# Kernel tuning notes

Hardware: AMD Instinct MI355X
Metric: run time of the kernel (lower is better)

Reference implementation:

```python
import jax, jax.numpy as jnp
import numpy as np

B, H, S = 64, 1024, 512
MIN_VAL, MAX_VAL = -1.0, 1.0
EPS = 1e-8  # torch F.cosine_similarity default eps


def setup_inputs() -> dict:
    key = jax.random.key(0)
    k1, k2, k3 = jax.random.split(key, 3)
    tree_state = jax.random.normal(k1, (B, H), dtype=jnp.float32)
    seq_states = jax.random.normal(k2, (B, H, S), dtype=jnp.float32)
    # binary validity mask (float, as it is multiplied in)
    seq_mask = (jax.random.uniform(k3, (B, S)) < 0.9).astype(jnp.float32)
    return {"tree_state": tree_state, "seq_states": seq_states, "seq_mask": seq_mask}


def reference(tree_state, seq_states, seq_mask):
    # scan over the seq axis; carry h: (B, H)
    xs = (jnp.transpose(seq_states, (2, 0, 1)), seq_mask.T)  # (S,B,H), (S,B)

    def step(h, x):
        s, m = x  # s: (B,H), m: (B,)
        dot = jnp.sum(h * s, axis=-1)  # (B,)
        denom = jnp.maximum(
            jnp.linalg.norm(h, axis=-1) * jnp.linalg.norm(s, axis=-1), EPS
        )
        cos = (dot / denom)[:, None]  # (B,1)
        h_new = jnp.clip(h + (s - h * cos) * m[:, None], MIN_VAL, MAX_VAL)
        return h_new, None

    h, _ = jax.lax.scan(step, tree_state, xs)
    return h
```

## Files before the change

### kernel.cpp

```cpp
#include <hip/hip_runtime.h>


#define NB 64
#define NH 1024
#define NS 512
#define EL 16

template <int CTRL>
__device__ __forceinline__ float dpp_add(float x) {
  int s = __builtin_amdgcn_update_dpp(0, __builtin_bit_cast(int, x), CTRL, 0xf,
                                      0xf, true);
  return x + __builtin_bit_cast(float, s);
}

__device__ __forceinline__ float readlane_f(float v, int lane) {
  return __builtin_bit_cast(
      float, __builtin_amdgcn_readlane(__builtin_bit_cast(int, v), lane));
}

__device__ __forceinline__ void wave_sum3(float& a, float& b, float& c) {
  a = dpp_add<0x111>(a); b = dpp_add<0x111>(b); c = dpp_add<0x111>(c);
  a = dpp_add<0x112>(a); b = dpp_add<0x112>(b); c = dpp_add<0x112>(c);
  a = dpp_add<0x114>(a); b = dpp_add<0x114>(b); c = dpp_add<0x114>(c);
  a = dpp_add<0x118>(a); b = dpp_add<0x118>(b); c = dpp_add<0x118>(c);
  a = dpp_add<0x142>(a); b = dpp_add<0x142>(b); c = dpp_add<0x142>(c);
  a = dpp_add<0x143>(a); b = dpp_add<0x143>(b); c = dpp_add<0x143>(c);
  a = readlane_f(a, 63);
  b = readlane_f(b, 63);
  c = readlane_f(c, 63);
}

__global__ __launch_bounds__(64, 1) void otsu_scan_kernel(
    const float* __restrict__ tree,
    const float* __restrict__ seq,
    const float* __restrict__ mask,
    float* __restrict__ out) {
  const int b = blockIdx.x;
  const int lane = threadIdx.x;

  const float* hrow = tree + b * NH + lane * EL;
  float h[EL];
#pragma unroll
  for (int i = 0; i < EL / 4; ++i) {
    float4 v = *(const float4*)(hrow + 4 * i);
    h[4 * i + 0] = v.x;
    h[4 * i + 1] = v.y;
    h[4 * i + 2] = v.z;
    h[4 * i + 3] = v.w;
  }

  float m8[8];
#pragma unroll
  for (int k = 0; k < 8; ++k) m8[k] = mask[b * NS + k * 64 + lane];

  const float* srow = seq + (size_t)b * NH * NS + (size_t)(lane * EL) * NS;

  float bufA[4 * EL], bufB[4 * EL];

  auto prefetch = [&](float* buf, int g) {
    const float* p = srow + 4 * g;
#pragma unroll
    for (int i = 0; i < EL; ++i) {
      float4 v = *(const float4*)(p + i * NS);
      buf[4 * i + 0] = v.x;
      buf[4 * i + 1] = v.y;
      buf[4 * i + 2] = v.z;
      buf[4 * i + 3] = v.w;
    }
    __builtin_amdgcn_sched_barrier(0);
  };

  auto full_step = [&](const float* buf, int j) {
    float d0 = 0.f, d1 = 0.f, d2 = 0.f, d3 = 0.f;
    float e0 = 0.f, e1 = 0.f, e2 = 0.f, e3 = 0.f;
    float f0 = 0.f, f1 = 0.f, f2 = 0.f, f3 = 0.f;
#pragma unroll
    for (int i = 0; i < EL; i += 4) {
      const float s0 = buf[4 * (i + 0) + j];
      const float s1 = buf[4 * (i + 1) + j];
      const float s2v = buf[4 * (i + 2) + j];
      const float s3 = buf[4 * (i + 3) + j];
      d0 = fmaf(h[i + 0], s0, d0);
      d1 = fmaf(h[i + 1], s1, d1);
      d2 = fmaf(h[i + 2], s2v, d2);
      d3 = fmaf(h[i + 3], s3, d3);
      e0 = fmaf(h[i + 0], h[i + 0], e0);
      e1 = fmaf(h[i + 1], h[i + 1], e1);
      e2 = fmaf(h[i + 2], h[i + 2], e2);
      e3 = fmaf(h[i + 3], h[i + 3], e3);
      f0 = fmaf(s0, s0, f0);
      f1 = fmaf(s1, s1, f1);
      f2 = fmaf(s2v, s2v, f2);
      f3 = fmaf(s3, s3, f3);
    }
    float dot = (d0 + d1) + (d2 + d3);
    float h2 = (e0 + e1) + (e2 + e3);
    float s2 = (f0 + f1) + (f2 + f3);
    wave_sum3(dot, h2, s2);
    const float denom = fmaxf(__builtin_amdgcn_sqrtf(h2 * s2), 1e-8f);
    const float c = dot * __builtin_amdgcn_rcpf(denom);
    const float a = 1.0f - c;
#pragma unroll
    for (int i = 0; i < EL; ++i) {
      h[i] = __builtin_amdgcn_fmed3f(fmaf(h[i], a, buf[4 * i + j]), -1.0f,
                                     1.0f);
    }
  };

  auto process = [&](const float* buf, float mvec, int lbase, bool has_t0) {
#pragma unroll
    for (int j = 0; j < 4; ++j) {
      const float m = readlane_f(mvec, lbase + j);
      if (m != 0.0f) {
        full_step(buf, j);
      } else if (has_t0 && j == 0) {
#pragma unroll
        for (int i = 0; i < EL; ++i)
          h[i] = __builtin_amdgcn_fmed3f(h[i], -1.0f, 1.0f);
      }
    }
  };

  prefetch(bufA, 0);

#pragma unroll
  for (int sg = 0; sg < 8; ++sg) {
    const float mvec = m8[sg];
    for (int gg = 0; gg < 16; gg += 2) {
      const int g = sg * 16 + gg;
      prefetch(bufB, g + 1);
      process(bufA, mvec, 4 * gg, sg == 0 && gg == 0);
      if (g + 2 < NS / 4) prefetch(bufA, g + 2);
      process(bufB, mvec, 4 * gg + 4, false);
    }
  }

  float* orow = out + b * NH + lane * EL;
#pragma unroll
  for (int i = 0; i < EL / 4; ++i) {
    float4 v;
    v.x = h[4 * i + 0];
    v.y = h[4 * i + 1];
    v.z = h[4 * i + 2];
    v.w = h[4 * i + 3];
    *(float4*)(orow + 4 * i) = v;
  }
}

extern "C" void kernel_launch(void* const* d_in, const int* in_sizes, int n_in,
                              void* d_out, int out_size, void* d_ws,
                              size_t ws_size, hipStream_t stream) {
  const float* tree = (const float*)d_in[0];
  const float* seq = (const float*)d_in[1];
  const float* mask = (const float*)d_in[2];
  float* out = (float*)d_out;
  otsu_scan_kernel<<<dim3(NB), dim3(64), 0, stream>>>(tree, seq, mask, out);
}
```

Before: 321.2 us.

## Hand-schedule global loads with inline asm and batch seq-norm reductions per group

Replaces compiler-generated prefetch with inline-asm dwordx4 loads carrying immediate offsets and explicit vmcnt waits, so one buffer's loads stay in flight while the other is processed. The squared norms of the four seq columns in a group are computed together and reduced in one four-way DPP reduction, taking that reduction off the per-step serial chain; each step now reduces only dot and |h|^2. The sqrt-plus-reciprocal becomes a single rsq with the eps clamp squared. The risks are fragile manual waitcnt accounting and a slightly different eps and rounding behaviour.

```diff
diff --git a/kernel.cpp b/kernel.cpp
--- a/kernel.cpp
+++ b/kernel.cpp
@@ -5,6 +5,8 @@
 #define NH 1024
 #define NS 512
 #define EL 16
+
+typedef float v4f __attribute__((ext_vector_type(4)));
 
 template <int CTRL>
 __device__ __forceinline__ float dpp_add(float x) {
@@ -18,17 +20,70 @@
       float, __builtin_amdgcn_readlane(__builtin_bit_cast(int, v), lane));
 }
 
-__device__ __forceinline__ void wave_sum3(float& a, float& b, float& c) {
-  a = dpp_add<0x111>(a); b = dpp_add<0x111>(b); c = dpp_add<0x111>(c);
-  a = dpp_add<0x112>(a); b = dpp_add<0x112>(b); c = dpp_add<0x112>(c);
-  a = dpp_add<0x114>(a); b = dpp_add<0x114>(b); c = dpp_add<0x114>(c);
-  a = dpp_add<0x118>(a); b = dpp_add<0x118>(b); c = dpp_add<0x118>(c);
-  a = dpp_add<0x142>(a); b = dpp_add<0x142>(b); c = dpp_add<0x142>(c);
-  a = dpp_add<0x143>(a); b = dpp_add<0x143>(b); c = dpp_add<0x143>(c);
+__device__ __forceinline__ void wave_sum2(float& a, float& b) {
+  a = dpp_add<0x111>(a); b = dpp_add<0x111>(b);
+  a = dpp_add<0x112>(a); b = dpp_add<0x112>(b);
+  a = dpp_add<0x114>(a); b = dpp_add<0x114>(b);
+  a = dpp_add<0x118>(a); b = dpp_add<0x118>(b);
+  a = dpp_add<0x142>(a); b = dpp_add<0x142>(b);
+  a = dpp_add<0x143>(a); b = dpp_add<0x143>(b);
+  a = readlane_f(a, 63);
+  b = readlane_f(b, 63);
+}
+
+__device__ __forceinline__ void wave_sum4(float& a, float& b, float& c,
+                                          float& d) {
+  a = dpp_add<0x111>(a); b = dpp_add<0x111>(b); c = dpp_add<0x111>(c); d = dpp_add<0x111>(d);
+  a = dpp_add<0x112>(a); b = dpp_add<0x112>(b); c = dpp_add<0x112>(c); d = dpp_add<0x112>(d);
+  a = dpp_add<0x114>(a); b = dpp_add<0x114>(b); c = dpp_add<0x114>(c); d = dpp_add<0x114>(d);
+  a = dpp_add<0x118>(a); b = dpp_add<0x118>(b); c = dpp_add<0x118>(c); d = dpp_add<0x118>(d);
+  a = dpp_add<0x142>(a); b = dpp_add<0x142>(b); c = dpp_add<0x142>(c); d = dpp_add<0x142>(d);
+  a = dpp_add<0x143>(a); b = dpp_add<0x143>(b); c = dpp_add<0x143>(c); d = dpp_add<0x143>(d);
   a = readlane_f(a, 63);
   b = readlane_f(b, 63);
   c = readlane_f(c, 63);
-}
+  d = readlane_f(d, 63);
+}
+
+#define GLD4(dst, p, OFFSTR)                                   \
+  asm volatile("global_load_dwordx4 %0, %1, off" OFFSTR        \
+               : "=v"(dst)                                     \
+               : "v"(p))
+#define GLD1(dst, p)                                           \
+  asm volatile("global_load_dword %0, %1, off" : "=v"(dst) : "v"(p))
+
+#define ISSUE16(buf)                       \
+  do {                                     \
+    GLD4(buf[0], p0, " offset:-4096");     \
+    GLD4(buf[1], p0, " offset:-2048");     \
+    GLD4(buf[2], p0, "");                  \
+    GLD4(buf[3], p0, " offset:2048");      \
+    GLD4(buf[4], p1, " offset:-4096");     \
+    GLD4(buf[5], p1, " offset:-2048");     \
+    GLD4(buf[6], p1, "");                  \
+    GLD4(buf[7], p1, " offset:2048");      \
+    GLD4(buf[8], p2, " offset:-4096");     \
+    GLD4(buf[9], p2, " offset:-2048");     \
+    GLD4(buf[10], p2, "");                 \
+    GLD4(buf[11], p2, " offset:2048");     \
+    GLD4(buf[12], p3, " offset:-4096");    \
+    GLD4(buf[13], p3, " offset:-2048");    \
+    GLD4(buf[14], p3, "");                 \
+    GLD4(buf[15], p3, " offset:2048");     \
+    p0 += 4; p1 += 4; p2 += 4; p3 += 4;    \
+  } while (0)
+
+#define WAITPIN(buf, N)                                             \
+  do {                                                              \
+    asm volatile("s_waitcnt vmcnt(" N ")"                           \
+                 : "+v"(buf[0]), "+v"(buf[1]), "+v"(buf[2]),        \
+                   "+v"(buf[3]), "+v"(buf[4]), "+v"(buf[5]),        \
+                   "+v"(buf[6]), "+v"(buf[7]));                     \
+    asm volatile("s_waitcnt vmcnt(" N ")"                           \
+                 : "+v"(buf[8]), "+v"(buf[9]), "+v"(buf[10]),       \
+                   "+v"(buf[11]), "+v"(buf[12]), "+v"(buf[13]),     \
+                   "+v"(buf[14]), "+v"(buf[15]));                   \
+  } while (0)
 
 __global__ __launch_bounds__(64, 1) void otsu_scan_kernel(
     const float* __restrict__ tree,
@@ -39,80 +94,97 @@
   const int lane = threadIdx.x;
 
   const float* hrow = tree + b * NH + lane * EL;
+  v4f hv[4];
+  GLD4(hv[0], hrow, "");
+  GLD4(hv[1], hrow, " offset:16");
+  GLD4(hv[2], hrow, " offset:32");
+  GLD4(hv[3], hrow, " offset:48");
+  float m8[8];
+  {
+    const float* mp = mask + b * NS + lane;
+    GLD1(m8[0], mp);
+    GLD1(m8[1], mp + 64);
+    GLD1(m8[2], mp + 128);
+    GLD1(m8[3], mp + 192);
+    GLD1(m8[4], mp + 256);
+    GLD1(m8[5], mp + 320);
+    GLD1(m8[6], mp + 384);
+    GLD1(m8[7], mp + 448);
+  }
+  asm volatile("s_waitcnt vmcnt(0)"
+               : "+v"(hv[0]), "+v"(hv[1]), "+v"(hv[2]), "+v"(hv[3]),
+                 "+v"(m8[0]), "+v"(m8[1]), "+v"(m8[2]), "+v"(m8[3]),
+                 "+v"(m8[4]), "+v"(m8[5]), "+v"(m8[6]), "+v"(m8[7]));
+
   float h[EL];
 #pragma unroll
-  for (int i = 0; i < EL / 4; ++i) {
-    float4 v = *(const float4*)(hrow + 4 * i);
-    h[4 * i + 0] = v.x;
-    h[4 * i + 1] = v.y;
-    h[4 * i + 2] = v.z;
-    h[4 * i + 3] = v.w;
-  }
-
-  float m8[8];
-#pragma unroll
-  for (int k = 0; k < 8; ++k) m8[k] = mask[b * NS + k * 64 + lane];
+  for (int k = 0; k < 4; ++k) {
+    h[4 * k + 0] = hv[k].x;
+    h[4 * k + 1] = hv[k].y;
+    h[4 * k + 2] = hv[k].z;
+    h[4 * k + 3] = hv[k].w;
+  }
 
   const float* srow = seq + (size_t)b * NH * NS + (size_t)(lane * EL) * NS;
-
-  float bufA[4 * EL], bufB[4 * EL];
-
-  auto prefetch = [&](float* buf, int g) {
-    const float* p = srow + 4 * g;
-#pragma unroll
-    for (int i = 0; i < EL; ++i) {
-      float4 v = *(const float4*)(p + i * NS);
-      buf[4 * i + 0] = v.x;
-      buf[4 * i + 1] = v.y;
-      buf[4 * i + 2] = v.z;
-      buf[4 * i + 3] = v.w;
+  const float* p0 = srow + 2 * NS;
+  const float* p1 = srow + 6 * NS;
+  const float* p2 = srow + 10 * NS;
+  const float* p3 = srow + 14 * NS;
+
+  v4f bufA[16], bufB[16];
+
+  auto process4 = [&](const v4f* buf, float mv, int lbase, bool has_t0) {
+    float fA0 = 0.f, fA1 = 0.f, fA2 = 0.f, fA3 = 0.f;
+    float fB0 = 0.f, fB1 = 0.f, fB2 = 0.f, fB3 = 0.f;
+#pragma unroll
+    for (int i = 0; i < EL; i += 2) {
+      fA0 = fmaf(buf[i][0], buf[i][0], fA0);
+      fA1 = fmaf(buf[i][1], buf[i][1], fA1);
+      fA2 = fmaf(buf[i][2], buf[i][2], fA2);
+      fA3 = fmaf(buf[i][3], buf[i][3], fA3);
+      fB0 = fmaf(buf[i + 1][0], buf[i + 1][0], fB0);
+      fB1 = fmaf(buf[i + 1][1], buf[i + 1][1], fB1);
+      fB2 = fmaf(buf[i + 1][2], buf[i + 1][2], fB2);
+      fB3 = fmaf(buf[i + 1][3], buf[i + 1][3], fB3);
     }
-    __builtin_amdgcn_sched_barrier(0);
-  };
-
-  auto full_step = [&](const float* buf, int j) {
-    float d0 = 0.f, d1 = 0.f, d2 = 0.f, d3 = 0.f;
-    float e0 = 0.f, e1 = 0.f, e2 = 0.f, e3 = 0.f;
-    float f0 = 0.f, f1 = 0.f, f2 = 0.f, f3 = 0.f;
-#pragma unroll
-    for (int i = 0; i < EL; i += 4) {
-      const float s0 = buf[4 * (i + 0) + j];
-      const float s1 = buf[4 * (i + 1) + j];
-      const float s2v = buf[4 * (i + 2) + j];
-      const float s3 = buf[4 * (i + 3) + j];
-      d0 = fmaf(h[i + 0], s0, d0);
-      d1 = fmaf(h[i + 1], s1, d1);
-      d2 = fmaf(h[i + 2], s2v, d2);
-      d3 = fmaf(h[i + 3], s3, d3);
-      e0 = fmaf(h[i + 0], h[i + 0], e0);
-      e1 = fmaf(h[i + 1], h[i + 1], e1);
-      e2 = fmaf(h[i + 2], h[i + 2], e2);
-      e3 = fmaf(h[i + 3], h[i + 3], e3);
-      f0 = fmaf(s0, s0, f0);
-      f1 = fmaf(s1, s1, f1);
-      f2 = fmaf(s2v, s2v, f2);
-      f3 = fmaf(s3, s3, f3);
-    }
-    float dot = (d0 + d1) + (d2 + d3);
-    float h2 = (e0 + e1) + (e2 + e3);
-    float s2 = (f0 + f1) + (f2 + f3);
-    wave_sum3(dot, h2, s2);
-    const float denom = fmaxf(__builtin_amdgcn_sqrtf(h2 * s2), 1e-8f);
-    const float c = dot * __builtin_amdgcn_rcpf(denom);
-    const float a = 1.0f - c;
-#pragma unroll
-    for (int i = 0; i < EL; ++i) {
-      h[i] = __builtin_amdgcn_fmed3f(fmaf(h[i], a, buf[4 * i + j]), -1.0f,
-                                     1.0f);
-    }
-  };
-
-  auto process = [&](const float* buf, float mvec, int lbase, bool has_t0) {
+    float s2g[4];
+    s2g[0] = fA0 + fB0;
+    s2g[1] = fA1 + fB1;
+    s2g[2] = fA2 + fB2;
+    s2g[3] = fA3 + fB3;
+    wave_sum4(s2g[0], s2g[1], s2g[2], s2g[3]);
+
 #pragma unroll
     for (int j = 0; j < 4; ++j) {
-      const float m = readlane_f(mvec, lbase + j);
+      const float m = readlane_f(mv, lbase + j);
       if (m != 0.0f) {
-        full_step(buf, j);
+        float d0 = 0.f, d1 = 0.f, d2 = 0.f, d3 = 0.f;
+        float e0 = 0.f, e1 = 0.f, e2 = 0.f, e3 = 0.f;
+#pragma unroll
+        for (int i = 0; i < EL; i += 4) {
+          const float sA = buf[i + 0][j];
+          const float sB = buf[i + 1][j];
+          const float sC = buf[i + 2][j];
+          const float sD = buf[i + 3][j];
+          d0 = fmaf(h[i + 0], sA, d0);
+          e0 = fmaf(h[i + 0], h[i + 0], e0);
+          d1 = fmaf(h[i + 1], sB, d1);
+          e1 = fmaf(h[i + 1], h[i + 1], e1);
+          d2 = fmaf(h[i + 2], sC, d2);
+          e2 = fmaf(h[i + 2], h[i + 2], e2);
+          d3 = fmaf(h[i + 3], sD, d3);
+          e3 = fmaf(h[i + 3], h[i + 3], e3);
+        }
+        float dot = (d0 + d1) + (d2 + d3);
+        float hh = (e0 + e1) + (e2 + e3);
+        wave_sum2(dot, hh);
+        const float p = fmaxf(hh * s2g[j], 1e-16f);
+        const float c = dot * __builtin_amdgcn_rsqf(p);
+        const float a = 1.0f - c;
+#pragma unroll
+        for (int i = 0; i < EL; ++i)
+          h[i] = __builtin_amdgcn_fmed3f(fmaf(h[i], a, buf[i][j]), -1.0f,
+                                         1.0f);
       } else if (has_t0 && j == 0) {
 #pragma unroll
         for (int i = 0; i < EL; ++i)
@@ -121,18 +193,29 @@
     }
   };
 
-  prefetch(bufA, 0);
+  ISSUE16(bufA);
 
 #pragma unroll
   for (int sg = 0; sg < 8; ++sg) {
-    const float mvec = m8[sg];
-    for (int gg = 0; gg < 16; gg += 2) {
-      const int g = sg * 16 + gg;
-      prefetch(bufB, g + 1);
-      process(bufA, mvec, 4 * gg, sg == 0 && gg == 0);
-      if (g + 2 < NS / 4) prefetch(bufA, g + 2);
-      process(bufB, mvec, 4 * gg + 4, false);
+    const float mv = m8[sg];
+    const int nIter = (sg == 7) ? 7 : 8;
+    for (int it = 0; it < nIter; ++it) {
+      const int lbase = 8 * it;
+      ISSUE16(bufB);
+      WAITPIN(bufA, "16");
+      process4(bufA, mv, lbase, sg == 0 && it == 0);
+      ISSUE16(bufA);
+      WAITPIN(bufB, "16");
+      process4(bufB, mv, lbase + 4, false);
     }
+  }
+  {
+    const float mv = m8[7];
+    ISSUE16(bufB);
+    WAITPIN(bufA, "16");
+    process4(bufA, mv, 56, false);
+    WAITPIN(bufB, "0");
+    process4(bufB, mv, 60, false);
   }
 
   float* orow = out + b * NH + lane * EL;
```

New measurement: 314.1 us. -2.2%, faster.
